# Performance work log

Hardware: AMD Instinct MI355X
Metric: run time of the kernel (lower is better)

## Reference

```python
import jax, jax.numpy as jnp
import numpy as np

OUT_H, OUT_W = 7, 7
SPATIAL_SCALE = 0.0625
N_IMG, C, H, W = 2, 256, 38, 38
NUM_ROIS = 256
IMG_MAX = 607.9  # keeps floor(coord*scale) <= 37


def setup_inputs() -> dict:
    key = jax.random.key(0)
    k_feat, k_b, k_xa, k_xb, k_ya, k_yb = jax.random.split(key, 6)
    feat = jax.random.normal(k_feat, (N_IMG, C, H, W), dtype=jnp.float32)
    bidx = jax.random.randint(k_b, (NUM_ROIS,), 0, N_IMG).astype(jnp.float32)
    xa = jax.random.uniform(k_xa, (NUM_ROIS,), minval=0.0, maxval=IMG_MAX)
    xb = jax.random.uniform(k_xb, (NUM_ROIS,), minval=0.0, maxval=IMG_MAX)
    ya = jax.random.uniform(k_ya, (NUM_ROIS,), minval=0.0, maxval=IMG_MAX)
    yb = jax.random.uniform(k_yb, (NUM_ROIS,), minval=0.0, maxval=IMG_MAX)
    rois = jnp.stack([bidx,
                      jnp.minimum(xa, xb), jnp.minimum(ya, yb),
                      jnp.maximum(xa, xb), jnp.maximum(ya, yb)], axis=1)
    return {"input": feat, "rois": rois.astype(jnp.float32)}


def _roi_max_pool(feat_all, rois):
    # feat_all: (N, C, H, W); rois: (R, 5) = (batch_idx, x1, y1, x2, y2)
    H_, W_ = feat_all.shape[2], feat_all.shape[3]
    b = rois[:, 0].astype(jnp.int32)
    # torch: rois[:,1:].mul_(scale); rois.long() -> truncation (== floor for >=0)
    coords = jnp.floor(rois[:, 1:] * SPATIAL_SCALE).astype(jnp.int32)
    x1, y1, x2, y2 = coords[:, 0], coords[:, 1], coords[:, 2], coords[:, 3]
    rh = y2 - y1 + 1  # inclusive crop: [y1, y2+1)
    rw = x2 - x1 + 1
    feat = feat_all[b]  # (R, C, H, W) per-ROI gather of its image
    neg = jnp.array(-jnp.inf, feat.dtype)

    # separable adaptive max pool: rows then cols
    hs = jnp.arange(H_)
    rows = []
    for i in range(OUT_H):  # fixed small loop over output bins
        hstart = y1 + (i * rh) // OUT_H                       # floor(i*rh/OUT_H)
        hend = y1 + ((i + 1) * rh + OUT_H - 1) // OUT_H       # ceil
        m = (hs[None, :] >= hstart[:, None]) & (hs[None, :] < hend[:, None])  # (R,H)
        rows.append(jnp.max(jnp.where(m[:, None, :, None], feat, neg), axis=2))  # (R,C,W)
    rowmax = jnp.stack(rows, axis=2)  # (R, C, OUT_H, W)

    ws = jnp.arange(W_)
    cols = []
    for j in range(OUT_W):
        wstart = x1 + (j * rw) // OUT_W
        wend = x1 + ((j + 1) * rw + OUT_W - 1) // OUT_W
        m = (ws[None, :] >= wstart[:, None]) & (ws[None, :] < wend[:, None])  # (R,W)
        cols.append(jnp.max(jnp.where(m[:, None, None, :], rowmax, neg), axis=3))  # (R,C,OUT_H)
    return jnp.stack(cols, axis=3)  # (R, C, OUT_H, OUT_W)


def reference(input, rois):
    return _roi_max_pool(input, rois)
```

## Files before the change

kernel.cpp:

```cpp
#include <hip/hip_runtime.h>
#include <math.h>

#define OUT_H 7
#define OUT_W 7
#define N_C 256
#define N_IMG 2
#define FH 38
#define FW 38
#define HW (FH * FW)
#define NUM_ROIS 256
#define N_OUT_POS (NUM_ROIS * OUT_H * OUT_W)
#define SPATIAL_SCALE 0.0625f

#define FEATT_FLOATS (N_IMG * HW * N_C)
#define OUTT_OFF FEATT_FLOATS

__global__ __launch_bounds__(256) void transpose_nchw_nhwc(
    const float* __restrict__ feat, float* __restrict__ featT)
{
    __shared__ float tile[64][65];
    const int bid = blockIdx.x;
    const int b   = bid / (23 * 4);
    const int rem = bid % (23 * 4);
    const int p0  = (rem / 4) * 64;
    const int c0  = (rem % 4) * 64;
    const int tx  = threadIdx.x & 63;
    const int tz  = threadIdx.x >> 6;

    const int p = p0 + tx;
    if (p < HW) {
        #pragma unroll
        for (int s = 0; s < 64; s += 4)
            tile[tz + s][tx] = feat[((size_t)(b * N_C + c0 + tz + s)) * HW + p];
    }
    __syncthreads();
    #pragma unroll
    for (int s = 0; s < 64; s += 4) {
        const int pp = p0 + tz + s;
        if (pp < HW)
            featT[((size_t)(b * HW + pp)) * N_C + c0 + tx] = tile[tx][tz + s];
    }
}

__global__ __launch_bounds__(256) void roi_pool_wavepos(
    const float* __restrict__ featT,
    const float* __restrict__ rois,
    float4* __restrict__ outT)
{
    const int lane = threadIdx.x & 63;
    const int wv   = threadIdx.x >> 6;
    const int g    = blockIdx.x * 4 + wv;
    const int r    = g / 49;
    const int ij   = g - r * 49;
    const int i    = ij / OUT_W;
    const int j    = ij - i * OUT_W;

    const float* roi = rois + (size_t)r * 5;
    const int b  = (int)roi[0];
    const int x1 = (int)(roi[1] * SPATIAL_SCALE);
    const int y1 = (int)(roi[2] * SPATIAL_SCALE);
    const int x2 = (int)(roi[3] * SPATIAL_SCALE);
    const int y2 = (int)(roi[4] * SPATIAL_SCALE);
    const int rh = y2 - y1 + 1;
    const int rw = x2 - x1 + 1;

    const int hs = y1 + (i * rh) / OUT_H;
    const int he = y1 + ((i + 1) * rh + OUT_H - 1) / OUT_H;
    const int ws = x1 + (j * rw) / OUT_W;
    const int we = x1 + ((j + 1) * rw + OUT_W - 1) / OUT_W;

    const float4* fb = (const float4*)featT + (size_t)b * HW * (N_C / 4) + lane;

    float4 m0 = make_float4(-INFINITY, -INFINITY, -INFINITY, -INFINITY);
    float4 m1 = m0;
    for (int h = hs; h < he; ++h) {
        const float4* rowp = fb + (size_t)(h * FW) * (N_C / 4);
        int w = ws;
        for (; w + 1 < we; w += 2) {
            const float4 v0 = rowp[(size_t)w * (N_C / 4)];
            const float4 v1 = rowp[(size_t)(w + 1) * (N_C / 4)];
            m0.x = fmaxf(m0.x, v0.x); m0.y = fmaxf(m0.y, v0.y);
            m0.z = fmaxf(m0.z, v0.z); m0.w = fmaxf(m0.w, v0.w);
            m1.x = fmaxf(m1.x, v1.x); m1.y = fmaxf(m1.y, v1.y);
            m1.z = fmaxf(m1.z, v1.z); m1.w = fmaxf(m1.w, v1.w);
        }
        if (w < we) {
            const float4 v0 = rowp[(size_t)w * (N_C / 4)];
            m0.x = fmaxf(m0.x, v0.x); m0.y = fmaxf(m0.y, v0.y);
            m0.z = fmaxf(m0.z, v0.z); m0.w = fmaxf(m0.w, v0.w);
        }
    }
    m0.x = fmaxf(m0.x, m1.x); m0.y = fmaxf(m0.y, m1.y);
    m0.z = fmaxf(m0.z, m1.z); m0.w = fmaxf(m0.w, m1.w);

    outT[(size_t)g * 64 + lane] = m0;
}

__global__ __launch_bounds__(256) void transpose_out(
    const float* __restrict__ outT, float* __restrict__ out)
{
    __shared__ float t[64][50];
    const int r   = blockIdx.x >> 2;
    const int c0  = (blockIdx.x & 3) * 64;
    const int tid = threadIdx.x;

    const float* src = outT + (size_t)r * 49 * N_C + c0;
    for (int k = tid; k < 49 * 64; k += 256) {
        const int ij = k >> 6;
        const int cl = k & 63;
        t[cl][ij] = src[(size_t)ij * N_C + cl];
    }
    __syncthreads();

    float* dst = out + ((size_t)r * N_C + c0) * 49;
    for (int k = tid; k < 64 * 49; k += 256) {
        const int cl = k / 49;
        const int ij = k - cl * 49;
        dst[(size_t)cl * 49 + ij] = t[cl][ij];
    }
}

extern "C" void kernel_launch(void* const* d_in, const int* in_sizes, int n_in,
                              void* d_out, int out_size, void* d_ws, size_t ws_size,
                              hipStream_t stream) {
    const float* feat = (const float*)d_in[0];
    const float* rois = (const float*)d_in[1];
    float* out   = (float*)d_out;
    float* featT = (float*)d_ws;
    float4* outT = (float4*)((float*)d_ws + OUTT_OFF);

    transpose_nchw_nhwc<<<N_IMG * 23 * 4, 256, 0, stream>>>(feat, featT);
    roi_pool_wavepos<<<N_OUT_POS / 4, 256, 0, stream>>>(featT, rois, outT);
    transpose_out<<<NUM_ROIS * 4, 256, 0, stream>>>((const float*)outT, out);
}
```

Measured before the change: 82.15 us.

## Fuse ROI pooling with output transpose via shared-memory staging per ROI

Each block now handles one whole ROI with 512 threads: its eight wavefronts loop over the 49 bins, write the channel maxima into a padded shared-memory tile, then store the ROI's NCHW output contiguously. This removes the separate output-transpose kernel, one launch, and the intermediate outT global write and read. In exchange the grid shrinks to 256 blocks, each using about 50KB of LDS, which lowers parallelism and occupancy on a large GPU. Load imbalance is also possible because bin sizes differ between ROIs.

```diff
diff --git a/kernel.cpp b/kernel.cpp
--- a/kernel.cpp
+++ b/kernel.cpp
@@ -9,11 +9,8 @@
 #define FW 38
 #define HW (FH * FW)
 #define NUM_ROIS 256
-#define N_OUT_POS (NUM_ROIS * OUT_H * OUT_W)
 #define SPATIAL_SCALE 0.0625f
-
-#define FEATT_FLOATS (N_IMG * HW * N_C)
-#define OUTT_OFF FEATT_FLOATS
+#define SPITCH 257
 
 __global__ __launch_bounds__(256) void transpose_nchw_nhwc(
     const float* __restrict__ feat, float* __restrict__ featT)
@@ -42,18 +39,16 @@
     }
 }
 
-__global__ __launch_bounds__(256) void roi_pool_wavepos(
+__global__ __launch_bounds__(512) void roi_pool_fused(
     const float* __restrict__ featT,
     const float* __restrict__ rois,
-    float4* __restrict__ outT)
+    float* __restrict__ out)
 {
+    __shared__ float s_out[49 * SPITCH];
+
+    const int r    = blockIdx.x;
     const int lane = threadIdx.x & 63;
     const int wv   = threadIdx.x >> 6;
-    const int g    = blockIdx.x * 4 + wv;
-    const int r    = g / 49;
-    const int ij   = g - r * 49;
-    const int i    = ij / OUT_W;
-    const int j    = ij - i * OUT_W;
 
     const float* roi = rois + (size_t)r * 5;
     const int b  = (int)roi[0];
@@ -64,59 +59,51 @@
     const int rh = y2 - y1 + 1;
     const int rw = x2 - x1 + 1;
 
-    const int hs = y1 + (i * rh) / OUT_H;
-    const int he = y1 + ((i + 1) * rh + OUT_H - 1) / OUT_H;
-    const int ws = x1 + (j * rw) / OUT_W;
-    const int we = x1 + ((j + 1) * rw + OUT_W - 1) / OUT_W;
-
     const float4* fb = (const float4*)featT + (size_t)b * HW * (N_C / 4) + lane;
 
-    float4 m0 = make_float4(-INFINITY, -INFINITY, -INFINITY, -INFINITY);
-    float4 m1 = m0;
-    for (int h = hs; h < he; ++h) {
-        const float4* rowp = fb + (size_t)(h * FW) * (N_C / 4);
-        int w = ws;
-        for (; w + 1 < we; w += 2) {
-            const float4 v0 = rowp[(size_t)w * (N_C / 4)];
-            const float4 v1 = rowp[(size_t)(w + 1) * (N_C / 4)];
-            m0.x = fmaxf(m0.x, v0.x); m0.y = fmaxf(m0.y, v0.y);
-            m0.z = fmaxf(m0.z, v0.z); m0.w = fmaxf(m0.w, v0.w);
-            m1.x = fmaxf(m1.x, v1.x); m1.y = fmaxf(m1.y, v1.y);
-            m1.z = fmaxf(m1.z, v1.z); m1.w = fmaxf(m1.w, v1.w);
+    for (int ij = wv; ij < OUT_H * OUT_W; ij += 8) {
+        const int i = ij / OUT_W;
+        const int j = ij - i * OUT_W;
+        const int hs = y1 + (i * rh) / OUT_H;
+        const int he = y1 + ((i + 1) * rh + OUT_H - 1) / OUT_H;
+        const int ws = x1 + (j * rw) / OUT_W;
+        const int we = x1 + ((j + 1) * rw + OUT_W - 1) / OUT_W;
+
+        float4 m0 = make_float4(-INFINITY, -INFINITY, -INFINITY, -INFINITY);
+        float4 m1 = m0;
+        for (int h = hs; h < he; ++h) {
+            const float4* rowp = fb + (size_t)(h * FW) * (N_C / 4);
+            int w = ws;
+            for (; w + 1 < we; w += 2) {
+                const float4 v0 = rowp[(size_t)w * (N_C / 4)];
+                const float4 v1 = rowp[(size_t)(w + 1) * (N_C / 4)];
+                m0.x = fmaxf(m0.x, v0.x); m0.y = fmaxf(m0.y, v0.y);
+                m0.z = fmaxf(m0.z, v0.z); m0.w = fmaxf(m0.w, v0.w);
+                m1.x = fmaxf(m1.x, v1.x); m1.y = fmaxf(m1.y, v1.y);
+                m1.z = fmaxf(m1.z, v1.z); m1.w = fmaxf(m1.w, v1.w);
+            }
+            if (w < we) {
+                const float4 v0 = rowp[(size_t)w * (N_C / 4)];
+                m0.x = fmaxf(m0.x, v0.x); m0.y = fmaxf(m0.y, v0.y);
+                m0.z = fmaxf(m0.z, v0.z); m0.w = fmaxf(m0.w, v0.w);
+            }
         }
-        if (w < we) {
-            const float4 v0 = rowp[(size_t)w * (N_C / 4)];
-            m0.x = fmaxf(m0.x, v0.x); m0.y = fmaxf(m0.y, v0.y);
-            m0.z = fmaxf(m0.z, v0.z); m0.w = fmaxf(m0.w, v0.w);
-        }
-    }
-    m0.x = fmaxf(m0.x, m1.x); m0.y = fmaxf(m0.y, m1.y);
-    m0.z = fmaxf(m0.z, m1.z); m0.w = fmaxf(m0.w, m1.w);
+        m0.x = fmaxf(m0.x, m1.x); m0.y = fmaxf(m0.y, m1.y);
+        m0.z = fmaxf(m0.z, m1.z); m0.w = fmaxf(m0.w, m1.w);
 
-    outT[(size_t)g * 64 + lane] = m0;
-}
-
-__global__ __launch_bounds__(256) void transpose_out(
-    const float* __restrict__ outT, float* __restrict__ out)
-{
-    __shared__ float t[64][50];
-    const int r   = blockIdx.x >> 2;
-    const int c0  = (blockIdx.x & 3) * 64;
-    const int tid = threadIdx.x;
-
-    const float* src = outT + (size_t)r * 49 * N_C + c0;
-    for (int k = tid; k < 49 * 64; k += 256) {
-        const int ij = k >> 6;
-        const int cl = k & 63;
-        t[cl][ij] = src[(size_t)ij * N_C + cl];
+        float* row = s_out + ij * SPITCH;
+        row[0 * 64 + lane] = m0.x;
+        row[1 * 64 + lane] = m0.y;
+        row[2 * 64 + lane] = m0.z;
+        row[3 * 64 + lane] = m0.w;
     }
     __syncthreads();
 
-    float* dst = out + ((size_t)r * N_C + c0) * 49;
-    for (int k = tid; k < 64 * 49; k += 256) {
-        const int cl = k / 49;
-        const int ij = k - cl * 49;
-        dst[(size_t)cl * 49 + ij] = t[cl][ij];
+    float* outr = out + (size_t)r * (N_C * 49);
+    for (int k = threadIdx.x; k < N_C * 49; k += 512) {
+        const int c  = k / 49;
+        const int ij = k - c * 49;
+        outr[k] = s_out[ij * SPITCH + (c & 3) * 64 + (c >> 2)];
     }
 }
 
@@ -127,9 +114,7 @@
     const float* rois = (const float*)d_in[1];
     float* out   = (float*)d_out;
     float* featT = (float*)d_ws;
-    float4* outT = (float4*)((float*)d_ws + OUTT_OFF);
 
     transpose_nchw_nhwc<<<N_IMG * 23 * 4, 256, 0, stream>>>(feat, featT);
-    roi_pool_wavepos<<<N_OUT_POS / 4, 256, 0, stream>>>(featT, rois, outT);
-    transpose_out<<<NUM_ROIS * 4, 256, 0, stream>>>((const float*)outT, out);
+    roi_pool_fused<<<NUM_ROIS, 512, 0, stream>>>(featT, rois, out);
 }
```

Result: slower. 92.42 us (+12.5%).
